# Performance work log

Hardware: AMD Instinct MI355X
Metric: run time of the kernel (lower is better)

Reference implementation:

```python
import jax, jax.numpy as jnp
import numpy as np

NUM_HEADS = 4
KEY_DIM = 8
WINDOW = 4
SHIFT = 2
CHANNELS = 32


def setup_inputs() -> dict:
    key = jax.random.key(0)
    ks = jax.random.split(key, 9)
    C, H, D = CHANNELS, NUM_HEADS, KEY_DIM
    s = 0.05
    return {
        "x": jax.random.normal(ks[0], (4, 512, 512, C), jnp.float32),
        "Wq": jax.random.normal(ks[1], (C, H, D), jnp.float32) * s,
        "bq": jax.random.normal(ks[2], (H, D), jnp.float32) * s,
        "Wk": jax.random.normal(ks[3], (C, H, D), jnp.float32) * s,
        "bk": jax.random.normal(ks[4], (H, D), jnp.float32) * s,
        "Wv": jax.random.normal(ks[5], (C, H, D), jnp.float32) * s,
        "bv": jax.random.normal(ks[6], (H, D), jnp.float32) * s,
        "Wo": jax.random.normal(ks[7], (H, D, C), jnp.float32) * s,
        "bo": jax.random.normal(ks[8], (C,), jnp.float32) * s,
    }


def reference(x, Wq, bq, Wk, bk, Wv, bv, Wo, bo):
    B, H, W, C = x.shape
    ws, sh = WINDOW, SHIFT
    pad_h = (ws - H % ws) % ws
    pad_w = (ws - W % ws) % ws
    p = jnp.pad(x, ((0, 0), (0, pad_h), (0, pad_w), (0, 0)))
    if sh:
        p = jnp.roll(p, shift=(-sh, -sh), axis=(1, 2))
    Hp, Wp = H + pad_h, W + pad_w
    hw, ww = Hp // ws, Wp // ws
    # partition into windows: [B*hw*ww, ws*ws, C]
    win = p.reshape(B, hw, ws, ww, ws, C).transpose(0, 1, 3, 2, 4, 5)
    win = win.reshape(-1, ws * ws, C)
    # multi-head self-attention within each window (Keras MultiHeadAttention math)
    q = jnp.einsum('bnc,chd->bnhd', win, Wq) + bq
    k = jnp.einsum('bnc,chd->bnhd', win, Wk) + bk
    v = jnp.einsum('bnc,chd->bnhd', win, Wv) + bv
    scores = jnp.einsum('bqhd,bkhd->bhqk', q, k) / np.sqrt(KEY_DIM).astype(np.float32)
    attn = jax.nn.softmax(scores, axis=-1)
    o = jnp.einsum('bhqk,bkhd->bqhd', attn, v)
    out = jnp.einsum('bqhd,hdc->bqc', o, Wo) + bo
    # merge windows back: [B, Hp, Wp, C]
    out = out.reshape(B, hw, ww, ws, ws, C).transpose(0, 1, 3, 2, 4, 5)
    out = out.reshape(B, Hp, Wp, C)
    if sh:
        out = jnp.roll(out, shift=(sh, sh), axis=(1, 2))
    out = out[:, :H, :W, :]
    return x + out
```

## Files before the change

### kernel.cpp

```cpp
#include <hip/hip_runtime.h>
#include <hip/hip_bf16.h>
#include <stdint.h>

typedef float f32x4 __attribute__((ext_vector_type(4)));
typedef short s16x8 __attribute__((ext_vector_type(8)));
typedef unsigned short u16;
typedef u16 u16x4 __attribute__((ext_vector_type(4)));

__device__ __forceinline__ u16 f2bf(float f) {
    union { __hip_bfloat16 h; u16 u; } cv;
    cv.h = __float2bfloat16(f);
    return cv.u;
}

__device__ __forceinline__ f32x4 mfma16(s16x8 a, s16x8 b, f32x4 c) {
    return __builtin_amdgcn_mfma_f32_16x16x32_bf16(a, b, c, 0, 0, 0);
}

#define LDS_FENCE() asm volatile("s_waitcnt lgkmcnt(0)" ::: "memory")

__global__ __launch_bounds__(256) void swin_attn_kernel(
    const float* __restrict__ x,
    const float* __restrict__ Wq, const float* __restrict__ bq,
    const float* __restrict__ Wk, const float* __restrict__ bk,
    const float* __restrict__ Wv, const float* __restrict__ bv,
    const float* __restrict__ Wo, const float* __restrict__ bo,
    float* __restrict__ out)
{
    const int lane  = threadIdx.x & 63;
    const int wave  = threadIdx.x >> 6;
    const int col16 = lane & 15;
    const int g     = lane >> 4;

    __shared__ __align__(16) u16 qk_bf[4][16][72];
    __shared__ __align__(16) u16 vT_bf[4][32][24];
    __shared__ __align__(16) u16 p_bf[4][16][24];
    __shared__ __align__(16) u16 o_bf[4][16][40];

    const float scale = 0.35355339059327373f;

    s16x8 wqkv[6];
    #pragma unroll
    for (int j = 0; j < 6; ++j) {
        const float* Wsrc = (j < 2) ? Wq : (j < 4) ? Wk : Wv;
        const int colW = ((j & 1) << 4) | col16;
        const float sc = (j < 2) ? scale : 1.0f;
        s16x8 wf;
        #pragma unroll
        for (int jj = 0; jj < 8; ++jj)
            wf[jj] = (short)f2bf(Wsrc[(g * 8 + jj) * 32 + colW] * sc);
        wqkv[j] = wf;
    }
    f32x4 bias_qk[4];
    #pragma unroll
    for (int j = 0; j < 4; ++j) {
        const float* bsrc = (j < 2) ? bq : bk;
        const float sc = (j < 2) ? scale : 1.0f;
        #pragma unroll
        for (int i = 0; i < 4; ++i)
            bias_qk[j][i] = bsrc[((j & 1) << 4) + 4 * g + i] * sc;
    }
    f32x4 bias_v[2];
    #pragma unroll
    for (int jv = 0; jv < 2; ++jv) {
        float b = bv[jv * 16 + col16];
        bias_v[jv] = (f32x4){b, b, b, b};
    }
    s16x8 wo_frag[2];
    f32x4 bo_frag[2];
    #pragma unroll
    for (int j2 = 0; j2 < 2; ++j2) {
        const int cout = j2 * 16 + col16;
        s16x8 wf;
        #pragma unroll
        for (int jj = 0; jj < 8; ++jj)
            wf[jj] = (short)f2bf(Wo[(g * 8 + jj) * 32 + cout]);
        wo_frag[j2] = wf;
        #pragma unroll
        for (int i = 0; i < 4; ++i)
            bo_frag[j2][i] = bo[j2 * 16 + 4 * g + i];
    }

    const f32x4 zero4 = {0.f, 0.f, 0.f, 0.f};
    const s16x8 zero8 = {0, 0, 0, 0, 0, 0, 0, 0};

    #pragma unroll 1
    for (int it = 0; it < 4; ++it) {
        const int w   = (blockIdx.x * 4 + wave) * 4 + it;
        const int b   = w >> 14;
        const int rem = w & 16383;
        const int wi  = rem >> 7;
        const int wj  = rem & 127;

        const int t    = col16;
        const int row  = (wi * 4 + (t >> 2) + 2) & 511;
        const int colp = (wj * 4 + (t & 3) + 2) & 511;
        const long pixbase = ((((long)b << 9) + row) * 512 + colp) * 32;

        f32x4 x0 = *(const f32x4*)(x + pixbase + g * 8);
        f32x4 x1 = *(const f32x4*)(x + pixbase + g * 8 + 4);
        s16x8 xfrag;
        #pragma unroll
        for (int i = 0; i < 4; ++i) {
            xfrag[i]     = (short)f2bf(x0[i]);
            xfrag[i + 4] = (short)f2bf(x1[i]);
        }

        #pragma unroll
        for (int j = 0; j < 4; ++j) {
            f32x4 c = mfma16(wqkv[j], xfrag, bias_qk[j]);
            u16x4 qv;
            #pragma unroll
            for (int i = 0; i < 4; ++i) qv[i] = f2bf(c[i]);
            *(u16x4*)&qk_bf[wave][col16][j * 16 + 4 * g] = qv;
        }
        #pragma unroll
        for (int jv = 0; jv < 2; ++jv) {
            f32x4 c = mfma16(xfrag, wqkv[4 + jv], bias_v[jv]);
            u16x4 vv;
            #pragma unroll
            for (int i = 0; i < 4; ++i) vv[i] = f2bf(c[i]);
            *(u16x4*)&vT_bf[wave][jv * 16 + col16][4 * g] = vv;
        }
        LDS_FENCE();

        #pragma unroll
        for (int h = 0; h < 4; ++h) {
            s16x8 afrag = zero8, bfrag = zero8;
            if (g == 0) {
                afrag = *(const s16x8*)&qk_bf[wave][col16][32 + h * 8];
                bfrag = *(const s16x8*)&qk_bf[wave][col16][h * 8];
            }
            f32x4 s = mfma16(afrag, bfrag, zero4);
            float p0 = __expf(s[0]);
            float p1 = __expf(s[1]);
            float p2 = __expf(s[2]);
            float p3 = __expf(s[3]);
            float sum = (p0 + p1) + (p2 + p3);
            sum += __shfl_xor(sum, 16);
            sum += __shfl_xor(sum, 32);
            const float inv = __builtin_amdgcn_rcpf(sum);
            u16x4 pv;
            pv[0] = f2bf(p0 * inv); pv[1] = f2bf(p1 * inv);
            pv[2] = f2bf(p2 * inv); pv[3] = f2bf(p3 * inv);
            *(u16x4*)&p_bf[wave][col16][4 * g] = pv;
            LDS_FENCE();

            s16x8 vfrag = zero8, pfrag = zero8;
            if (g < 2) {
                vfrag = *(const s16x8*)&vT_bf[wave][h * 8 + (col16 & 7)][g * 8];
                pfrag = *(const s16x8*)&p_bf[wave][col16][g * 8];
            }
            f32x4 oc = mfma16(vfrag, pfrag, zero4);
            if (g < 2) {
                u16x4 ov;
                #pragma unroll
                for (int i = 0; i < 4; ++i) ov[i] = f2bf(oc[i]);
                *(u16x4*)&o_bf[wave][col16][h * 8 + 4 * g] = ov;
            }
            LDS_FENCE();
        }

        s16x8 ofrag = *(const s16x8*)&o_bf[wave][col16][g * 8];
        #pragma unroll
        for (int j2 = 0; j2 < 2; ++j2) {
            f32x4 c = mfma16(wo_frag[j2], ofrag, bo_frag[j2]);
            f32x4 r = *(const f32x4*)(x + pixbase + j2 * 16 + 4 * g);
            #pragma unroll
            for (int i = 0; i < 4; ++i) c[i] += r[i];
            *(f32x4*)(out + pixbase + j2 * 16 + 4 * g) = c;
        }
        LDS_FENCE();
    }
}

extern "C" void kernel_launch(void* const* d_in, const int* in_sizes, int n_in,
                              void* d_out, int out_size, void* d_ws, size_t ws_size,
                              hipStream_t stream) {
    const float* x  = (const float*)d_in[0];
    const float* Wq = (const float*)d_in[1];
    const float* bq = (const float*)d_in[2];
    const float* Wk = (const float*)d_in[3];
    const float* bk = (const float*)d_in[4];
    const float* Wv = (const float*)d_in[5];
    const float* bv = (const float*)d_in[6];
    const float* Wo = (const float*)d_in[7];
    const float* bo = (const float*)d_in[8];
    float* out = (float*)d_out;

    dim3 grid(4096), block(256);
    hipLaunchKernelGGL(swin_attn_kernel, grid, block, 0, stream,
                       x, Wq, bq, Wk, bk, Wv, bv, Wo, bo, out);
}
```

Before: 64.84 us.

## Prefetch next window input, batch per-head softmax, use native exp2

Loads the next window's input pixels during the current iteration, and issues the residual reads early so global-memory latency overlaps with compute. Splits the per-head loop into separate score, softmax and PV phases, with a per-head P buffer, so the LDS waits drop from two per head to one per phase. Folds log2(e) into the Q scale so the hardware v_exp_f32 (exp2) replaces __expf. It also drops the trailing LDS fence, which adds a redundant wraparound prefetch on the last iteration and raises LDS usage and register pressure.

```diff
diff --git a/kernel.cpp b/kernel.cpp
--- a/kernel.cpp
+++ b/kernel.cpp
@@ -12,11 +12,12 @@
     cv.h = __float2bfloat16(f);
     return cv.u;
 }
-
 __device__ __forceinline__ f32x4 mfma16(s16x8 a, s16x8 b, f32x4 c) {
     return __builtin_amdgcn_mfma_f32_16x16x32_bf16(a, b, c, 0, 0, 0);
 }
-
+__device__ __forceinline__ float exp2_hw(float x) {
+    float r; asm("v_exp_f32 %0, %1" : "=v"(r) : "v"(x)); return r;
+}
 #define LDS_FENCE() asm volatile("s_waitcnt lgkmcnt(0)" ::: "memory")
 
 __global__ __launch_bounds__(256) void swin_attn_kernel(
@@ -34,17 +35,18 @@
 
     __shared__ __align__(16) u16 qk_bf[4][16][72];
     __shared__ __align__(16) u16 vT_bf[4][32][24];
-    __shared__ __align__(16) u16 p_bf[4][16][24];
+    __shared__ __align__(16) u16 p_bf[4][4][16][24];
     __shared__ __align__(16) u16 o_bf[4][16][40];
 
-    const float scale = 0.35355339059327373f;
+    const float scale  = 0.35355339059327373f;
+    const float qscale = scale * 1.4426950408889634f;
 
     s16x8 wqkv[6];
     #pragma unroll
     for (int j = 0; j < 6; ++j) {
         const float* Wsrc = (j < 2) ? Wq : (j < 4) ? Wk : Wv;
         const int colW = ((j & 1) << 4) | col16;
-        const float sc = (j < 2) ? scale : 1.0f;
+        const float sc = (j < 2) ? qscale : 1.0f;
         s16x8 wf;
         #pragma unroll
         for (int jj = 0; jj < 8; ++jj)
@@ -55,7 +57,7 @@
     #pragma unroll
     for (int j = 0; j < 4; ++j) {
         const float* bsrc = (j < 2) ? bq : bk;
-        const float sc = (j < 2) ? scale : 1.0f;
+        const float sc = (j < 2) ? qscale : 1.0f;
         #pragma unroll
         for (int i = 0; i < 4; ++i)
             bias_qk[j][i] = bsrc[((j & 1) << 4) + 4 * g + i] * sc;
@@ -84,27 +86,28 @@
     const f32x4 zero4 = {0.f, 0.f, 0.f, 0.f};
     const s16x8 zero8 = {0, 0, 0, 0, 0, 0, 0, 0};
 
+    const int wbase = (blockIdx.x * 4 + wave) * 4;
+    long curpix;
+    f32x4 px0, px1;
+    {
+        const int w = wbase;
+        const int b = w >> 14, rem = w & 16383, wi = rem >> 7, wj = rem & 127;
+        const int row  = (wi * 4 + (col16 >> 2) + 2) & 511;
+        const int colp = (wj * 4 + (col16 & 3) + 2) & 511;
+        curpix = ((((long)b << 9) + row) * 512 + colp) * 32;
+        px0 = *(const f32x4*)(x + curpix + g * 8);
+        px1 = *(const f32x4*)(x + curpix + g * 8 + 4);
+    }
+
     #pragma unroll 1
     for (int it = 0; it < 4; ++it) {
-        const int w   = (blockIdx.x * 4 + wave) * 4 + it;
-        const int b   = w >> 14;
-        const int rem = w & 16383;
-        const int wi  = rem >> 7;
-        const int wj  = rem & 127;
-
-        const int t    = col16;
-        const int row  = (wi * 4 + (t >> 2) + 2) & 511;
-        const int colp = (wj * 4 + (t & 3) + 2) & 511;
-        const long pixbase = ((((long)b << 9) + row) * 512 + colp) * 32;
-
-        f32x4 x0 = *(const f32x4*)(x + pixbase + g * 8);
-        f32x4 x1 = *(const f32x4*)(x + pixbase + g * 8 + 4);
         s16x8 xfrag;
         #pragma unroll
         for (int i = 0; i < 4; ++i) {
-            xfrag[i]     = (short)f2bf(x0[i]);
-            xfrag[i + 4] = (short)f2bf(x1[i]);
-        }
+            xfrag[i]     = (short)f2bf(px0[i]);
+            xfrag[i + 4] = (short)f2bf(px1[i]);
+        }
+        const long pixbase = curpix;
 
         #pragma unroll
         for (int j = 0; j < 4; ++j) {
@@ -122,8 +125,23 @@
             for (int i = 0; i < 4; ++i) vv[i] = f2bf(c[i]);
             *(u16x4*)&vT_bf[wave][jv * 16 + col16][4 * g] = vv;
         }
+
+        {
+            const int w = wbase + ((it + 1) & 3);
+            const int b = w >> 14, rem = w & 16383, wi = rem >> 7, wj = rem & 127;
+            const int row  = (wi * 4 + (col16 >> 2) + 2) & 511;
+            const int colp = (wj * 4 + (col16 & 3) + 2) & 511;
+            const long np = ((((long)b << 9) + row) * 512 + colp) * 32;
+            px0 = *(const f32x4*)(x + np + g * 8);
+            px1 = *(const f32x4*)(x + np + g * 8 + 4);
+            curpix = np;
+        }
+        f32x4 r0 = *(const f32x4*)(x + pixbase + 4 * g);
+        f32x4 r1 = *(const f32x4*)(x + pixbase + 16 + 4 * g);
+
         LDS_FENCE();
 
+        f32x4 s[4];
         #pragma unroll
         for (int h = 0; h < 4; ++h) {
             s16x8 afrag = zero8, bfrag = zero8;
@@ -131,11 +149,14 @@
                 afrag = *(const s16x8*)&qk_bf[wave][col16][32 + h * 8];
                 bfrag = *(const s16x8*)&qk_bf[wave][col16][h * 8];
             }
-            f32x4 s = mfma16(afrag, bfrag, zero4);
-            float p0 = __expf(s[0]);
-            float p1 = __expf(s[1]);
-            float p2 = __expf(s[2]);
-            float p3 = __expf(s[3]);
+            s[h] = mfma16(afrag, bfrag, zero4);
+        }
+        #pragma unroll
+        for (int h = 0; h < 4; ++h) {
+            float p0 = exp2_hw(s[h][0]);
+            float p1 = exp2_hw(s[h][1]);
+            float p2 = exp2_hw(s[h][2]);
+            float p3 = exp2_hw(s[h][3]);
             float sum = (p0 + p1) + (p2 + p3);
             sum += __shfl_xor(sum, 16);
             sum += __shfl_xor(sum, 32);
@@ -143,13 +164,16 @@
             u16x4 pv;
             pv[0] = f2bf(p0 * inv); pv[1] = f2bf(p1 * inv);
             pv[2] = f2bf(p2 * inv); pv[3] = f2bf(p3 * inv);
-            *(u16x4*)&p_bf[wave][col16][4 * g] = pv;
-            LDS_FENCE();
-
+            *(u16x4*)&p_bf[wave][h][col16][4 * g] = pv;
+        }
+        LDS_FENCE();
+
+        #pragma unroll
+        for (int h = 0; h < 4; ++h) {
             s16x8 vfrag = zero8, pfrag = zero8;
             if (g < 2) {
                 vfrag = *(const s16x8*)&vT_bf[wave][h * 8 + (col16 & 7)][g * 8];
-                pfrag = *(const s16x8*)&p_bf[wave][col16][g * 8];
+                pfrag = *(const s16x8*)&p_bf[wave][h][col16][g * 8];
             }
             f32x4 oc = mfma16(vfrag, pfrag, zero4);
             if (g < 2) {
@@ -158,19 +182,22 @@
                 for (int i = 0; i < 4; ++i) ov[i] = f2bf(oc[i]);
                 *(u16x4*)&o_bf[wave][col16][h * 8 + 4 * g] = ov;
             }
-            LDS_FENCE();
-        }
+        }
+        LDS_FENCE();
 
         s16x8 ofrag = *(const s16x8*)&o_bf[wave][col16][g * 8];
-        #pragma unroll
-        for (int j2 = 0; j2 < 2; ++j2) {
-            f32x4 c = mfma16(wo_frag[j2], ofrag, bo_frag[j2]);
-            f32x4 r = *(const f32x4*)(x + pixbase + j2 * 16 + 4 * g);
-            #pragma unroll
-            for (int i = 0; i < 4; ++i) c[i] += r[i];
-            *(f32x4*)(out + pixbase + j2 * 16 + 4 * g) = c;
-        }
-        LDS_FENCE();
+        {
+            f32x4 c = mfma16(wo_frag[0], ofrag, bo_frag[0]);
+            #pragma unroll
+            for (int i = 0; i < 4; ++i) c[i] += r0[i];
+            *(f32x4*)(out + pixbase + 4 * g) = c;
+        }
+        {
+            f32x4 c = mfma16(wo_frag[1], ofrag, bo_frag[1]);
+            #pragma unroll
+            for (int i = 0; i < 4; ++i) c[i] += r1[i];
+            *(f32x4*)(out + pixbase + 16 + 4 * g) = c;
+        }
     }
 }
 
```

After: 64.65 us. No clear change (-0.3%).
